# Kernel optimization log

Hardware: AMD Instinct MI355X
Metric: run time of the kernel (lower is better)

The kernel has to match this reference:

```python
import jax, jax.numpy as jnp
import numpy as np

N, E = 50000, 600000
IN, H, C = 128, 8, 32
HC = H * C
LAT, OUT, NCOM = 32, 64, 30
BN_EPS = 1e-5
NEG_SLOPE = 0.2


def setup_inputs() -> dict:
    key = jax.random.key(0)
    ks = jax.random.split(key, 32)
    f32 = jnp.float32
    def rn(i, shape, s=0.05):
        return jax.random.normal(ks[i], shape, f32) * s
    inp = {
        'x': jax.random.normal(ks[0], (N, IN), f32),
        'eps': jax.random.normal(ks[1], (N, LAT), f32),
        'edge_index': jax.random.randint(ks[2], (2, E), 0, N, jnp.int32),
        # GAT layer 1 (in -> H*C)
        'gat1_W': rn(3, (IN, HC)), 'gat1_asrc': rn(4, (H, C)), 'gat1_adst': rn(5, (H, C)), 'gat1_b': jnp.zeros((HC,), f32),
        'bn1_g': jnp.ones((HC,), f32), 'bn1_b': jnp.zeros((HC,), f32),
        # GAT layer 2 (H*C -> H*C)
        'gat2_W': rn(6, (HC, HC)), 'gat2_asrc': rn(7, (H, C)), 'gat2_adst': rn(8, (H, C)), 'gat2_b': jnp.zeros((HC,), f32),
        'bn2_g': jnp.ones((HC,), f32), 'bn2_b': jnp.zeros((HC,), f32),
        # GAT layer 3 (H*C -> H*C)
        'gat3_W': rn(9, (HC, HC)), 'gat3_asrc': rn(10, (H, C)), 'gat3_adst': rn(11, (H, C)), 'gat3_b': jnp.zeros((HC,), f32),
        'bn3_g': jnp.ones((HC,), f32), 'bn3_b': jnp.zeros((HC,), f32),
        # heads
        'res_W': rn(12, (IN, HC)), 'res_b': jnp.zeros((HC,), f32),
        'mu_W': rn(13, (HC, LAT)), 'mu_b': jnp.zeros((LAT,), f32),
        'lv_W': rn(14, (HC, LAT)), 'lv_b': jnp.zeros((LAT,), f32),
        'dec_W': rn(15, (LAT, OUT)), 'dec_b': jnp.zeros((OUT,), f32),
        'aux_W': rn(16, (HC, NCOM)), 'aux_b': jnp.zeros((NCOM,), f32),
    }
    return inp


def gat_conv(x, src, dst, W, asrc, adst, b):
    # PyG GATConv (concat=True, self-loops already in src/dst, lin bias=False)
    n = x.shape[0]
    h = (x @ W).reshape(n, H, C)                      # [N,H,C]
    a_s = jnp.einsum('nhc,hc->nh', h, asrc)           # [N,H]
    a_d = jnp.einsum('nhc,hc->nh', h, adst)
    e = jax.nn.leaky_relu(a_s[src] + a_d[dst], NEG_SLOPE)  # [E,H]
    m = jax.ops.segment_max(e, dst, num_segments=n)        # per-dest softmax (stable)
    p = jnp.exp(e - m[dst])
    s = jax.ops.segment_sum(p, dst, num_segments=n)
    alpha = p / (s[dst] + 1e-16)                      # [E,H]
    out = jax.ops.segment_sum(h[src] * alpha[:, :, None], dst, num_segments=n)
    return out.reshape(n, HC) + b


def batch_norm(x, g, b):
    mu = x.mean(0)
    var = x.var(0)  # biased var, as torch BN uses for normalization
    return (x - mu) * jax.lax.rsqrt(var + BN_EPS) * g + b


def reference(x, eps, edge_index,
              gat1_W, gat1_asrc, gat1_adst, gat1_b, bn1_g, bn1_b,
              gat2_W, gat2_asrc, gat2_adst, gat2_b, bn2_g, bn2_b,
              gat3_W, gat3_asrc, gat3_adst, gat3_b, bn3_g, bn3_b,
              res_W, res_b, mu_W, mu_b, lv_W, lv_b, dec_W, dec_b, aux_W, aux_b):
    loops = jnp.arange(N, dtype=edge_index.dtype)
    src = jnp.concatenate([edge_index[0], loops])
    dst = jnp.concatenate([edge_index[1], loops])

    residual = x @ res_W + res_b
    h = jax.nn.relu(batch_norm(gat_conv(x, src, dst, gat1_W, gat1_asrc, gat1_adst, gat1_b), bn1_g, bn1_b))
    h = jax.nn.relu(batch_norm(gat_conv(h, src, dst, gat2_W, gat2_asrc, gat2_adst, gat2_b), bn2_g, bn2_b))
    h = jax.nn.relu(batch_norm(gat_conv(h, src, dst, gat3_W, gat3_asrc, gat3_adst, gat3_b), bn3_g, bn3_b))
    h = h + residual

    mu = h @ mu_W + mu_b
    logvar = h @ lv_W + lv_b
    z = mu + eps * jnp.exp(0.5 * logvar)   # reparameterize
    out = z @ dec_W + dec_b
    aux = h @ aux_W + aux_b
    return (out, mu, logvar, aux)
```

## Files before the change

### kernel.cpp

```cpp
#include <hip/hip_runtime.h>

#define N_NODES 50000
#define N_EDGES 600000
#define HC 256
#define NH 8
#define AGG_BLOCKS 2048
#define AGG_WAVES (AGG_BLOCKS * 4)

typedef short s8v __attribute__((ext_vector_type(8)));
typedef float f4v __attribute__((ext_vector_type(4)));
typedef _Float16 h4v __attribute__((ext_vector_type(4)));
typedef __attribute__((address_space(1))) const unsigned int as1_cu32;
typedef __attribute__((address_space(3))) unsigned int as3_u32;

__device__ inline ushort f2bf(float f) {
  unsigned u = __float_as_uint(f);
  unsigned r = u + 0x7FFF + ((u >> 16) & 1);
  return (ushort)(r >> 16);
}

__global__ void k_init_cnt(int* __restrict__ cnt) {
  int i = blockIdx.x * 256 + threadIdx.x;
  if (i < N_NODES) cnt[i] = 1;
}

__global__ void k_count(const int* __restrict__ dstE, int* __restrict__ cnt) {
  int e = blockIdx.x * 256 + threadIdx.x;
  if (e < N_EDGES) atomicAdd(&cnt[dstE[e]], 1);
}

__global__ void k_scan_bsum(const int* __restrict__ cnt, int* __restrict__ bsum) {
  __shared__ int sd[256];
  int i = blockIdx.x * 256 + threadIdx.x;
  sd[threadIdx.x] = (i < N_NODES) ? cnt[i] : 0;
  __syncthreads();
  for (int o = 128; o > 0; o >>= 1) {
    if (threadIdx.x < o) sd[threadIdx.x] += sd[threadIdx.x + o];
    __syncthreads();
  }
  if (threadIdx.x == 0) bsum[blockIdx.x] = sd[0];
}

__global__ void k_scan_offsets(int* __restrict__ bsum, int nb) {
  __shared__ int s[256];
  int t = threadIdx.x;
  int v = (t < nb) ? bsum[t] : 0;
  s[t] = v; __syncthreads();
  for (int o = 1; o < 256; o <<= 1) {
    int x = (t >= o) ? s[t - o] : 0;
    __syncthreads();
    s[t] += x;
    __syncthreads();
  }
  if (t < nb) bsum[t] = s[t] - v;
}

__global__ void k_scan_write(const int* __restrict__ cnt, const int* __restrict__ bsum,
                             int* __restrict__ rowptr, int* __restrict__ fillptr) {
  __shared__ int s[256];
  int t = threadIdx.x;
  int i = blockIdx.x * 256 + t;
  int v = (i < N_NODES) ? cnt[i] : 0;
  s[t] = v; __syncthreads();
  for (int o = 1; o < 256; o <<= 1) {
    int x = (t >= o) ? s[t - o] : 0;
    __syncthreads();
    s[t] += x;
    __syncthreads();
  }
  int excl = s[t] - v + bsum[blockIdx.x];
  if (i < N_NODES) {
    rowptr[i] = excl;
    fillptr[i] = excl;
    if (i == N_NODES - 1) rowptr[N_NODES] = excl + v;
  }
}

__global__ void k_fill(const int* __restrict__ srcE, const int* __restrict__ dstE,
                       int* __restrict__ fillptr, int* __restrict__ srcs) {
  int i = blockIdx.x * 256 + threadIdx.x;
  if (i < N_NODES) {
    int pos = atomicAdd(&fillptr[i], 1);
    srcs[pos] = i;
  } else if (i < N_NODES + N_EDGES) {
    int e = i - N_NODES;
    int pos = atomicAdd(&fillptr[dstE[e]], 1);
    srcs[pos] = srcE[e];
  }
}

__global__ void k_cvt_x(const float* __restrict__ X, ushort* __restrict__ Xb) {
  size_t i = ((size_t)blockIdx.x * 256 + threadIdx.x) * 4;
  float4 x4 = *(const float4*)&X[i];
  ushort4 o;
  o.x = f2bf(x4.x); o.y = f2bf(x4.y); o.z = f2bf(x4.z); o.w = f2bf(x4.w);
  *(ushort4*)&Xb[i] = o;
}

__global__ void k_cvt_wt(const float* __restrict__ W, ushort* __restrict__ Wt, int K, int Nw) {
  __shared__ ushort s[32][33];
  int tx = threadIdx.x & 31, ty = threadIdx.x >> 5;
  int k0 = blockIdx.x * 32, n0 = blockIdx.y * 32;
  for (int j = 0; j < 32; j += 8)
    s[ty + j][tx] = f2bf(W[(size_t)(k0 + ty + j) * Nw + n0 + tx]);
  __syncthreads();
  for (int j = 0; j < 32; j += 8)
    Wt[(size_t)(n0 + ty + j) * K + k0 + tx] = s[tx][ty + j];
}

__global__ void k_pack_head(const float* __restrict__ muW, const float* __restrict__ lvW,
                            const float* __restrict__ auxW, ushort* __restrict__ Wth) {
  int n = blockIdx.x;
  int k = threadIdx.x;
  float v = 0.f;
  if (n < 32) v = muW[k * 32 + n];
  else if (n < 64) v = lvW[k * 32 + (n - 32)];
  else if (n < 94) v = auxW[k * 30 + (n - 64)];
  Wth[n * 256 + k] = f2bf(v);
}

template <typename OutT>
__launch_bounds__(256)
__global__ void k_gemm_bf16(const ushort* __restrict__ A, const ushort* __restrict__ Wt,
                            const float* __restrict__ bias, OutT* __restrict__ Out,
                            int M, int K, int ldc) {
  __shared__ __align__(16) ushort As[16 * 512];
  __shared__ __align__(16) ushort Bs[16 * 512];
  int t = threadIdx.x, w = t >> 6, L = t & 63;
  int bm = blockIdx.x * 128, bn = blockIdx.y * 128;
  int lrow = L & 15, lcol = (L >> 4) * 8;

  const ushort* ga[4];
  const ushort* gb[4];
#pragma unroll
  for (int u = 0; u < 4; u++) {
    int i = w * 4 + u;
    int mt = i >> 1, ks = i & 1;
    int arow = bm + mt * 16 + lrow;
    if (arow >= M) arow = M - 1;
    ga[u] = A + (size_t)arow * K + ks * 32 + lcol;
    int brow = bn + mt * 16 + lrow;
    gb[u] = Wt + (size_t)brow * K + ks * 32 + lcol;
  }

  f4v acc[4][4];
  f4v zero = {0.f, 0.f, 0.f, 0.f};
#pragma unroll
  for (int mi = 0; mi < 4; mi++)
#pragma unroll
    for (int ni = 0; ni < 4; ni++) acc[mi][ni] = zero;

  int wm = (w >> 1) * 4;
  int wn = (w & 1) * 4;

  int nk = K >> 6;
  for (int kt = 0; kt < nk; kt++) {
#pragma unroll
    for (int u = 0; u < 4; u++) {
      int i = w * 4 + u;
      __builtin_amdgcn_global_load_lds((as1_cu32*)ga[u], (as3_u32*)&As[i * 512], 16, 0, 0);
      __builtin_amdgcn_global_load_lds((as1_cu32*)gb[u], (as3_u32*)&Bs[i * 512], 16, 0, 0);
      ga[u] += 64; gb[u] += 64;
    }
    __syncthreads();
#pragma unroll
    for (int ks = 0; ks < 2; ks++) {
      s8v af[4], bf[4];
#pragma unroll
      for (int mi = 0; mi < 4; mi++)
        af[mi] = *(const s8v*)&As[(((wm + mi) * 2 + ks) * 64 + L) * 8];
#pragma unroll
      for (int ni = 0; ni < 4; ni++)
        bf[ni] = *(const s8v*)&Bs[(((wn + ni) * 2 + ks) * 64 + L) * 8];
#pragma unroll
      for (int mi = 0; mi < 4; mi++)
#pragma unroll
        for (int ni = 0; ni < 4; ni++)
          acc[mi][ni] = __builtin_amdgcn_mfma_f32_16x16x32_bf16(af[mi], bf[ni], acc[mi][ni], 0, 0, 0);
    }
    __syncthreads();
  }
#pragma unroll
  for (int ni = 0; ni < 4; ni++) {
    int col = bn + (wn + ni) * 16 + (L & 15);
    float bb = bias ? bias[col] : 0.f;
#pragma unroll
    for (int mi = 0; mi < 4; mi++) {
      int rbase = bm + (wm + mi) * 16 + (L >> 4) * 4;
#pragma unroll
      for (int i = 0; i < 4; i++) {
        int r = rbase + i;
        if (r < M) Out[(size_t)r * ldc + col] = (OutT)(acc[mi][ni][i] + bb);
      }
    }
  }
}

__launch_bounds__(256)
__global__ void k_att(const _Float16* __restrict__ B, const float* __restrict__ asrc,
                      const float* __restrict__ adst,
                      float* __restrict__ as_, float* __restrict__ ad_) {
  int wid = (blockIdx.x * 256 + threadIdx.x) >> 6;
  int lane = threadIdx.x & 63;
  h4v x = *(const h4v*)&B[(size_t)wid * 256 + (lane << 2)];
  float4 s4 = *(const float4*)&asrc[lane << 2];
  float4 d4 = *(const float4*)&adst[lane << 2];
  float x0 = (float)x[0], x1 = (float)x[1], x2 = (float)x[2], x3 = (float)x[3];
  float vs = x0 * s4.x + x1 * s4.y + x2 * s4.z + x3 * s4.w;
  float vd = x0 * d4.x + x1 * d4.y + x2 * d4.z + x3 * d4.w;
  vs += __shfl_xor(vs, 1); vs += __shfl_xor(vs, 2); vs += __shfl_xor(vs, 4);
  vd += __shfl_xor(vd, 1); vd += __shfl_xor(vd, 2); vd += __shfl_xor(vd, 4);
  if ((lane & 7) == 0) {
    as_[wid * NH + (lane >> 3)] = vs;
    ad_[wid * NH + (lane >> 3)] = vd;
  }
}

__launch_bounds__(256)
__global__ void k_agg(const int* __restrict__ rowptr, const int* __restrict__ srcs,
                      const float* __restrict__ as_, const float* __restrict__ ad_,
                      const _Float16* __restrict__ B, const float* __restrict__ gb,
                      _Float16* __restrict__ C, float* __restrict__ part,
                      float* __restrict__ stats) {
  __shared__ float ss[4 * 512];
  int t = threadIdx.x;
  if (blockIdx.x == 0) {
    stats[t] = 0.f; stats[t + 256] = 0.f;
  }
  int w = t >> 6, lane = t & 63;
  int h = lane >> 3;
  int cb = lane << 2;
  float4 g4 = *(const float4*)&gb[cb];
  float sts0 = 0.f, sts1 = 0.f, sts2 = 0.f, sts3 = 0.f;
  float stq0 = 0.f, stq1 = 0.f, stq2 = 0.f, stq3 = 0.f;

  for (int n = blockIdx.x * 4 + w; n < N_NODES; n += AGG_WAVES) {
    int beg = rowptr[n], end = rowptr[n + 1];
    float ad_nh = ad_[n * NH + h];
    float ac0 = 0.f, ac1 = 0.f, ac2 = 0.f, ac3 = 0.f, wsum = 0.f;
    int k = beg;
    for (; k + 4 <= end; k += 4) {
      int s0 = srcs[k], s1 = srcs[k + 1], s2 = srcs[k + 2], s3 = srcs[k + 3];
      h4v b0 = *(const h4v*)&B[(size_t)s0 * 256 + cb];
      h4v b1 = *(const h4v*)&B[(size_t)s1 * 256 + cb];
      h4v b2 = *(const h4v*)&B[(size_t)s2 * 256 + cb];
      h4v b3 = *(const h4v*)&B[(size_t)s3 * 256 + cb];
      float e0 = as_[s0 * NH + h] + ad_nh; e0 = e0 > 0.f ? e0 : 0.2f * e0;
      float e1 = as_[s1 * NH + h] + ad_nh; e1 = e1 > 0.f ? e1 : 0.2f * e1;
      float e2 = as_[s2 * NH + h] + ad_nh; e2 = e2 > 0.f ? e2 : 0.2f * e2;
      float e3 = as_[s3 * NH + h] + ad_nh; e3 = e3 > 0.f ? e3 : 0.2f * e3;
      float p0 = __expf(e0), p1 = __expf(e1), p2 = __expf(e2), p3 = __expf(e3);
      wsum += (p0 + p1) + (p2 + p3);
      ac0 += p0 * (float)b0[0] + p1 * (float)b1[0] + p2 * (float)b2[0] + p3 * (float)b3[0];
      ac1 += p0 * (float)b0[1] + p1 * (float)b1[1] + p2 * (float)b2[1] + p3 * (float)b3[1];
      ac2 += p0 * (float)b0[2] + p1 * (float)b1[2] + p2 * (float)b2[2] + p3 * (float)b3[2];
      ac3 += p0 * (float)b0[3] + p1 * (float)b1[3] + p2 * (float)b2[3] + p3 * (float)b3[3];
    }
    for (; k < end; k++) {
      int s = srcs[k];
      h4v b4 = *(const h4v*)&B[(size_t)s * 256 + cb];
      float e = as_[s * NH + h] + ad_nh;
      e = e > 0.f ? e : 0.2f * e;
      float p = __expf(e);
      wsum += p;
      ac0 += p * (float)b4[0]; ac1 += p * (float)b4[1];
      ac2 += p * (float)b4[2]; ac3 += p * (float)b4[3];
    }
    float inv = 1.f / (wsum + 1e-16f);
    float v0 = ac0 * inv + g4.x, v1 = ac1 * inv + g4.y;
    float v2 = ac2 * inv + g4.z, v3 = ac3 * inv + g4.w;
    h4v o; o[0] = (_Float16)v0; o[1] = (_Float16)v1; o[2] = (_Float16)v2; o[3] = (_Float16)v3;
    *(h4v*)&C[(size_t)n * 256 + cb] = o;
    sts0 += v0; stq0 += v0 * v0;
    sts1 += v1; stq1 += v1 * v1;
    sts2 += v2; stq2 += v2 * v2;
    sts3 += v3; stq3 += v3 * v3;
  }
  float* sw = &ss[w * 512];
  sw[cb + 0] = sts0; sw[cb + 1] = sts1; sw[cb + 2] = sts2; sw[cb + 3] = sts3;
  sw[256 + cb + 0] = stq0; sw[256 + cb + 1] = stq1;
  sw[256 + cb + 2] = stq2; sw[256 + cb + 3] = stq3;
  __syncthreads();
  float p0 = ss[t] + ss[512 + t] + ss[1024 + t] + ss[1536 + t];
  float p1 = ss[256 + t] + ss[768 + t] + ss[1280 + t] + ss[1792 + t];
  part[(size_t)blockIdx.x * 512 + t] = p0;
  part[(size_t)blockIdx.x * 512 + 256 + t] = p1;
}

__global__ void k_bn_reduce(const float* __restrict__ part, float* __restrict__ stats) {
  int i = threadIdx.x;
  int base = blockIdx.x * (AGG_BLOCKS / 16);
  float s0 = 0.f, s1 = 0.f;
  for (int b = 0; b < AGG_BLOCKS / 16; b++) {
    s0 += part[(size_t)(base + b) * 512 + i];
    s1 += part[(size_t)(base + b) * 512 + 256 + i];
  }
  atomicAdd(&stats[i], s0);
  atomicAdd(&stats[256 + i], s1);
}

__global__ void k_bn_relu_cvt(const _Float16* __restrict__ X, const float* __restrict__ stats,
                              const float* __restrict__ g, const float* __restrict__ b,
                              const _Float16* __restrict__ resid, ushort* __restrict__ Xb) {
  size_t i = ((size_t)blockIdx.x * 256 + threadIdx.x) * 4;
  int c = (int)(i & 255);
  const float invN = 1.f / (float)N_NODES;
  h4v x4 = *(const h4v*)&X[i];
  float4 s4 = *(const float4*)&stats[c];
  float4 q4 = *(const float4*)&stats[256 + c];
  float4 g4 = *(const float4*)&g[c];
  float4 b4 = *(const float4*)&b[c];
  float m0 = s4.x * invN, m1 = s4.y * invN, m2 = s4.z * invN, m3 = s4.w * invN;
  float v0 = ((float)x4[0] - m0) * rsqrtf(q4.x * invN - m0 * m0 + 1e-5f) * g4.x + b4.x;
  float v1 = ((float)x4[1] - m1) * rsqrtf(q4.y * invN - m1 * m1 + 1e-5f) * g4.y + b4.y;
  float v2 = ((float)x4[2] - m2) * rsqrtf(q4.z * invN - m2 * m2 + 1e-5f) * g4.z + b4.z;
  float v3 = ((float)x4[3] - m3) * rsqrtf(q4.w * invN - m3 * m3 + 1e-5f) * g4.w + b4.w;
  v0 = v0 > 0.f ? v0 : 0.f; v1 = v1 > 0.f ? v1 : 0.f;
  v2 = v2 > 0.f ? v2 : 0.f; v3 = v3 > 0.f ? v3 : 0.f;
  if (resid) {
    h4v r4 = *(const h4v*)&resid[i];
    v0 += (float)r4[0]; v1 += (float)r4[1]; v2 += (float)r4[2]; v3 += (float)r4[3];
  }
  ushort4 ob;
  ob.x = f2bf(v0); ob.y = f2bf(v1); ob.z = f2bf(v2); ob.w = f2bf(v3);
  *(ushort4*)&Xb[i] = ob;
}

__launch_bounds__(256)
__global__ void k_dec(const _Float16* __restrict__ Hd, const float* __restrict__ eps,
                      const float* __restrict__ mub, const float* __restrict__ lvb,
                      const float* __restrict__ auxb,
                      const float* __restrict__ decW, const float* __restrict__ decb,
                      float* __restrict__ out) {
  __shared__ float wsd[2048];
  __shared__ float shz[4][32];
  int t = threadIdx.x;
  for (int i = t; i < 2048; i += 256) wsd[i] = decW[i];
  int w = t >> 6, lane = t & 63;
  int n = blockIdx.x * 4 + w;
  const _Float16* hd = &Hd[(size_t)n * 128];
  if (lane < 32) {
    float mu = (float)hd[lane] + mub[lane];
    float lv = (float)hd[32 + lane] + lvb[lane];
    out[(size_t)N_NODES * 64 + (size_t)n * 32 + lane] = mu;
    out[(size_t)N_NODES * 96 + (size_t)n * 32 + lane] = lv;
    shz[w][lane] = mu + eps[(size_t)n * 32 + lane] * __expf(0.5f * lv);
  } else if (lane < 62) {
    int j = lane - 32;
    out[(size_t)N_NODES * 128 + (size_t)n * 30 + j] = (float)hd[64 + j] + auxb[j];
  }
  __syncthreads();
  float o = decb[lane];
#pragma unroll 8
  for (int k = 0; k < 32; k++) o += shz[w][k] * wsd[k * 64 + lane];
  out[(size_t)n * 64 + lane] = o;
}

extern "C" void kernel_launch(void* const* d_in, const int* in_sizes, int n_in,
                              void* d_out, int out_size, void* d_ws, size_t ws_size,
                              hipStream_t stream) {
  (void)in_sizes; (void)n_in; (void)out_size; (void)ws_size;
  const float* x    = (const float*)d_in[0];
  const float* eps  = (const float*)d_in[1];
  const int*   ei   = (const int*)d_in[2];
  const float* gW[3]    = {(const float*)d_in[3],  (const float*)d_in[9],  (const float*)d_in[15]};
  const float* gasrc[3] = {(const float*)d_in[4],  (const float*)d_in[10], (const float*)d_in[16]};
  const float* gadst[3] = {(const float*)d_in[5],  (const float*)d_in[11], (const float*)d_in[17]};
  const float* gbias[3] = {(const float*)d_in[6],  (const float*)d_in[12], (const float*)d_in[18]};
  const float* bng[3]   = {(const float*)d_in[7],  (const float*)d_in[13], (const float*)d_in[19]};
  const float* bnb[3]   = {(const float*)d_in[8],  (const float*)d_in[14], (const float*)d_in[20]};
  const float* resW = (const float*)d_in[21];
  const float* resb = (const float*)d_in[22];
  const float* muW  = (const float*)d_in[23];
  const float* mub  = (const float*)d_in[24];
  const float* lvW  = (const float*)d_in[25];
  const float* lvb  = (const float*)d_in[26];
  const float* decW = (const float*)d_in[27];
  const float* decb = (const float*)d_in[28];
  const float* auxW = (const float*)d_in[29];
  const float* auxb = (const float*)d_in[30];
  float* out = (float*)d_out;

  char* ws = (char*)d_ws;
  size_t off = 0;
  auto alloc = [&](size_t bytes) -> void* {
    void* p = ws + off;
    off += (bytes + 255) & ~(size_t)255;
    return p;
  };
  _Float16* X0  = (_Float16*)alloc((size_t)N_NODES * HC * 2);
  _Float16* X1  = (_Float16*)alloc((size_t)N_NODES * HC * 2);
  _Float16* Rr  = (_Float16*)alloc((size_t)N_NODES * HC * 2);
  _Float16* Hd  = (_Float16*)alloc((size_t)N_NODES * 128 * 2);
  ushort* Xb    = (ushort*)alloc((size_t)N_NODES * HC * 2);
  float*  as_   = (float*)alloc((size_t)N_NODES * NH * 4);
  float*  ad_   = (float*)alloc((size_t)N_NODES * NH * 4);
  float*  stats = (float*)alloc(512 * 4);
  float*  part  = (float*)alloc((size_t)AGG_BLOCKS * 512 * 4);
  int* cnt      = (int*)alloc((size_t)N_NODES * 4);
  int* rowptr   = (int*)alloc((size_t)(N_NODES + 1) * 4);
  int* fillptr  = (int*)alloc((size_t)N_NODES * 4);
  int* srcs     = (int*)alloc((size_t)(N_NODES + N_EDGES) * 4);
  int* bsum     = (int*)alloc(256 * 4);
  ushort* Wt1   = (ushort*)alloc(256 * 128 * 2);
  ushort* Wt2   = (ushort*)alloc(256 * 256 * 2);
  ushort* Wt3   = (ushort*)alloc(256 * 256 * 2);
  ushort* WtR   = (ushort*)alloc(256 * 128 * 2);
  ushort* Wth   = (ushort*)alloc(128 * 256 * 2);

  const int NB = (N_NODES + 255) / 256;
  k_init_cnt<<<NB, 256, 0, stream>>>(cnt);
  k_count<<<(N_EDGES + 255) / 256, 256, 0, stream>>>(ei + N_EDGES, cnt);
  k_scan_bsum<<<NB, 256, 0, stream>>>(cnt, bsum);
  k_scan_offsets<<<1, 256, 0, stream>>>(bsum, NB);
  k_scan_write<<<NB, 256, 0, stream>>>(cnt, bsum, rowptr, fillptr);
  k_fill<<<(N_NODES + N_EDGES + 255) / 256, 256, 0, stream>>>(ei, ei + N_EDGES, fillptr, srcs);

  k_cvt_wt<<<dim3(4, 8), 256, 0, stream>>>(gW[0], Wt1, 128, 256);
  k_cvt_wt<<<dim3(8, 8), 256, 0, stream>>>(gW[1], Wt2, 256, 256);
  k_cvt_wt<<<dim3(8, 8), 256, 0, stream>>>(gW[2], Wt3, 256, 256);
  k_cvt_wt<<<dim3(4, 8), 256, 0, stream>>>(resW, WtR, 128, 256);
  k_pack_head<<<128, 256, 0, stream>>>(muW, lvW, auxW, Wth);
  k_cvt_x<<<(N_NODES * 128) / 1024, 256, 0, stream>>>(x, Xb);

  const int GM = (N_NODES + 127) / 128;
  k_gemm_bf16<_Float16><<<dim3(GM, 2), 256, 0, stream>>>(Xb, WtR, resb, Rr, N_NODES, 128, 256);

  const ushort* Wts[3] = {Wt1, Wt2, Wt3};
  int K = 128;
  for (int L = 0; L < 3; L++) {
    k_gemm_bf16<_Float16><<<dim3(GM, 2), 256, 0, stream>>>(Xb, Wts[L], nullptr, X0, N_NODES, K, 256);
    k_att<<<N_NODES / 4, 256, 0, stream>>>(X0, gasrc[L], gadst[L], as_, ad_);
    k_agg<<<AGG_BLOCKS, 256, 0, stream>>>(rowptr, srcs, as_, ad_, X0, gbias[L], X1, part, stats);
    k_bn_reduce<<<16, 256, 0, stream>>>(part, stats);
    k_bn_relu_cvt<<<(N_NODES * HC) / 1024, 256, 0, stream>>>(
        X1, stats, bng[L], bnb[L], (L == 2) ? Rr : nullptr, Xb);
    K = 256;
  }
  k_gemm_bf16<_Float16><<<dim3(GM, 1), 256, 0, stream>>>(Xb, Wth, nullptr, Hd, N_NODES, 256, 128);
  k_dec<<<N_NODES / 4, 256, 0, stream>>>(Hd, eps, mub, lvb, auxb, decW, decb, out);
}
```

Measured before the change: 653.4 us.

## Cooperatively compute edge softmax weights across lanes, broadcast via readlane/shuffle in GAT aggregation

The aggregation loop now processes 8 edges at a time. Each lane loads one (edge, head) source index and attention score, computes its exp weight once, then shares the source index with readlane and the weight with a shuffle. Before, every lane redundantly loaded srcs and as_ and computed exp for each edge. The fp16-to-fp32 multiply-accumulate also uses inline v_fma_mix_f32 instead of separate converts. In exchange it adds cross-lane traffic, a masked tail path, and inline asm that may block compiler scheduling.

```diff
diff --git a/kernel.cpp b/kernel.cpp
--- a/kernel.cpp
+++ b/kernel.cpp
@@ -229,6 +229,8 @@
   }
   int w = t >> 6, lane = t & 63;
   int h = lane >> 3;
+  int j = lane >> 3;
+  int hh = lane & 7;
   int cb = lane << 2;
   float4 g4 = *(const float4*)&gb[cb];
   float sts0 = 0.f, sts1 = 0.f, sts2 = 0.f, sts3 = 0.f;
@@ -236,35 +238,54 @@
 
   for (int n = blockIdx.x * 4 + w; n < N_NODES; n += AGG_WAVES) {
     int beg = rowptr[n], end = rowptr[n + 1];
-    float ad_nh = ad_[n * NH + h];
+    float ad_h = ad_[n * NH + hh];
     float ac0 = 0.f, ac1 = 0.f, ac2 = 0.f, ac3 = 0.f, wsum = 0.f;
     int k = beg;
-    for (; k + 4 <= end; k += 4) {
-      int s0 = srcs[k], s1 = srcs[k + 1], s2 = srcs[k + 2], s3 = srcs[k + 3];
-      h4v b0 = *(const h4v*)&B[(size_t)s0 * 256 + cb];
-      h4v b1 = *(const h4v*)&B[(size_t)s1 * 256 + cb];
-      h4v b2 = *(const h4v*)&B[(size_t)s2 * 256 + cb];
-      h4v b3 = *(const h4v*)&B[(size_t)s3 * 256 + cb];
-      float e0 = as_[s0 * NH + h] + ad_nh; e0 = e0 > 0.f ? e0 : 0.2f * e0;
-      float e1 = as_[s1 * NH + h] + ad_nh; e1 = e1 > 0.f ? e1 : 0.2f * e1;
-      float e2 = as_[s2 * NH + h] + ad_nh; e2 = e2 > 0.f ? e2 : 0.2f * e2;
-      float e3 = as_[s3 * NH + h] + ad_nh; e3 = e3 > 0.f ? e3 : 0.2f * e3;
-      float p0 = __expf(e0), p1 = __expf(e1), p2 = __expf(e2), p3 = __expf(e3);
-      wsum += (p0 + p1) + (p2 + p3);
-      ac0 += p0 * (float)b0[0] + p1 * (float)b1[0] + p2 * (float)b2[0] + p3 * (float)b3[0];
-      ac1 += p0 * (float)b0[1] + p1 * (float)b1[1] + p2 * (float)b2[1] + p3 * (float)b3[1];
-      ac2 += p0 * (float)b0[2] + p1 * (float)b1[2] + p2 * (float)b2[2] + p3 * (float)b3[2];
-      ac3 += p0 * (float)b0[3] + p1 * (float)b1[3] + p2 * (float)b2[3] + p3 * (float)b3[3];
-    }
-    for (; k < end; k++) {
-      int s = srcs[k];
-      h4v b4 = *(const h4v*)&B[(size_t)s * 256 + cb];
-      float e = as_[s * NH + h] + ad_nh;
+    for (; k + 8 <= end; k += 8) {
+      int s = srcs[k + j];
+      float e = as_[s * NH + hh] + ad_h;
       e = e > 0.f ? e : 0.2f * e;
       float p = __expf(e);
-      wsum += p;
-      ac0 += p * (float)b4[0]; ac1 += p * (float)b4[1];
-      ac2 += p * (float)b4[2]; ac3 += p * (float)b4[3];
+#pragma unroll
+      for (int jj = 0; jj < 8; jj++) {
+        int sj = __builtin_amdgcn_readlane(s, jj * 8);
+        float pj = __shfl(p, jj * 8 + h);
+        uint2 b2 = *(const uint2*)(B + (size_t)sj * 256 + cb);
+        wsum += pj;
+        asm("v_fma_mix_f32 %0, %1, %2, %0 op_sel:[0,0,0] op_sel_hi:[0,1,0]"
+            : "+v"(ac0) : "v"(pj), "v"(b2.x));
+        asm("v_fma_mix_f32 %0, %1, %2, %0 op_sel:[0,1,0] op_sel_hi:[0,1,0]"
+            : "+v"(ac1) : "v"(pj), "v"(b2.x));
+        asm("v_fma_mix_f32 %0, %1, %2, %0 op_sel:[0,0,0] op_sel_hi:[0,1,0]"
+            : "+v"(ac2) : "v"(pj), "v"(b2.y));
+        asm("v_fma_mix_f32 %0, %1, %2, %0 op_sel:[0,1,0] op_sel_hi:[0,1,0]"
+            : "+v"(ac3) : "v"(pj), "v"(b2.y));
+      }
+    }
+    if (k < end) {
+      int rem = end - k;
+      int idx = k + j; if (idx >= end) idx = end - 1;
+      int s = srcs[idx];
+      float e = as_[s * NH + hh] + ad_h;
+      e = e > 0.f ? e : 0.2f * e;
+      float p = (j < rem) ? __expf(e) : 0.f;
+#pragma unroll
+      for (int jj = 0; jj < 8; jj++) {
+        if (jj < rem) {
+          int sj = __builtin_amdgcn_readlane(s, jj * 8);
+          float pj = __shfl(p, jj * 8 + h);
+          uint2 b2 = *(const uint2*)(B + (size_t)sj * 256 + cb);
+          wsum += pj;
+          asm("v_fma_mix_f32 %0, %1, %2, %0 op_sel:[0,0,0] op_sel_hi:[0,1,0]"
+              : "+v"(ac0) : "v"(pj), "v"(b2.x));
+          asm("v_fma_mix_f32 %0, %1, %2, %0 op_sel:[0,1,0] op_sel_hi:[0,1,0]"
+              : "+v"(ac1) : "v"(pj), "v"(b2.x));
+          asm("v_fma_mix_f32 %0, %1, %2, %0 op_sel:[0,0,0] op_sel_hi:[0,1,0]"
+              : "+v"(ac2) : "v"(pj), "v"(b2.y));
+          asm("v_fma_mix_f32 %0, %1, %2, %0 op_sel:[0,1,0] op_sel_hi:[0,1,0]"
+              : "+v"(ac3) : "v"(pj), "v"(b2.y));
+        }
+      }
     }
     float inv = 1.f / (wsum + 1e-16f);
     float v0 = ac0 * inv + g4.x, v1 = ac1 * inv + g4.y;
```

Result: slower. 680.2 us (+4.1%).

## Precompute per-edge attention exponentials in separate kernel and use fma_mix in aggregation

Applied to the files above, without the earlier changes.

Adds a k_pre kernel that computes leaky-relu and exp attention weights for every edge and head, storing them in an edge-major p32 buffer laid out in groups of four edges. The aggregation loop then loads four weights with one vector load and accumulates with v_fma_mix_f32 inline asm on packed fp16 features, so it no longer converts fp16 to fp32 separately or computes exp inline. The aim is to cut the ALU work and scattered as_ gathers in the latency-bound gather loop. The cost is an extra kernel launch per layer and writing and reading a roughly 21 MB fp32 weight buffer.

```diff
diff --git a/kernel.cpp b/kernel.cpp
--- a/kernel.cpp
+++ b/kernel.cpp
@@ -217,9 +217,44 @@
 }
 
 __launch_bounds__(256)
+__global__ void k_pre(const int* __restrict__ rowptr, const int* __restrict__ srcs,
+                      const float* __restrict__ as_, const float* __restrict__ ad_,
+                      float* __restrict__ p32) {
+  int t = threadIdx.x;
+  int w = t >> 6, lane = t & 63;
+  int h = lane >> 3, j = lane & 7;
+  int jb = j & 4;
+  int jl = j & 3;
+  for (int n = blockIdx.x * 4 + w; n < N_NODES; n += AGG_WAVES) {
+    int beg = rowptr[n], end = rowptr[n + 1];
+    float adh = ad_[n * NH + h];
+    for (int k = beg; k + 4 <= end; k += 8) {
+      if (k + jb + 4 <= end) {
+        int e = k + j;
+        int s = srcs[e];
+        float v = as_[s * NH + h] + adh;
+        v = v > 0.f ? v : 0.2f * v;
+        p32[(size_t)8 * (k + jb) + h * 4 + jl] = __expf(v);
+      }
+    }
+  }
+}
+
+#define FMA4(P, B2)                                                                        \
+  asm("v_fma_mix_f32 %0, %1, %2, %0 op_sel:[0,0,0] op_sel_hi:[0,1,0]"                      \
+      : "+v"(ac0) : "v"(P), "v"((B2).x));                                                  \
+  asm("v_fma_mix_f32 %0, %1, %2, %0 op_sel:[0,1,0] op_sel_hi:[0,1,0]"                      \
+      : "+v"(ac1) : "v"(P), "v"((B2).x));                                                  \
+  asm("v_fma_mix_f32 %0, %1, %2, %0 op_sel:[0,0,0] op_sel_hi:[0,1,0]"                      \
+      : "+v"(ac2) : "v"(P), "v"((B2).y));                                                  \
+  asm("v_fma_mix_f32 %0, %1, %2, %0 op_sel:[0,1,0] op_sel_hi:[0,1,0]"                      \
+      : "+v"(ac3) : "v"(P), "v"((B2).y));
+
+__launch_bounds__(256)
 __global__ void k_agg(const int* __restrict__ rowptr, const int* __restrict__ srcs,
                       const float* __restrict__ as_, const float* __restrict__ ad_,
-                      const _Float16* __restrict__ B, const float* __restrict__ gb,
+                      const float* __restrict__ p32, const _Float16* __restrict__ B,
+                      const float* __restrict__ gb,
                       _Float16* __restrict__ C, float* __restrict__ part,
                       float* __restrict__ stats) {
   __shared__ float ss[4 * 512];
@@ -230,6 +265,7 @@
   int w = t >> 6, lane = t & 63;
   int h = lane >> 3;
   int cb = lane << 2;
+  const uint2* Bu = (const uint2*)B;
   float4 g4 = *(const float4*)&gb[cb];
   float sts0 = 0.f, sts1 = 0.f, sts2 = 0.f, sts3 = 0.f;
   float stq0 = 0.f, stq1 = 0.f, stq2 = 0.f, stq3 = 0.f;
@@ -238,23 +274,20 @@
     int beg = rowptr[n], end = rowptr[n + 1];
     float ad_nh = ad_[n * NH + h];
     float ac0 = 0.f, ac1 = 0.f, ac2 = 0.f, ac3 = 0.f, wsum = 0.f;
+    f4v wv = {0.f, 0.f, 0.f, 0.f};
     int k = beg;
     for (; k + 4 <= end; k += 4) {
+      f4v p4 = *(const f4v*)&p32[(size_t)8 * k + h * 4];
       int s0 = srcs[k], s1 = srcs[k + 1], s2 = srcs[k + 2], s3 = srcs[k + 3];
-      h4v b0 = *(const h4v*)&B[(size_t)s0 * 256 + cb];
-      h4v b1 = *(const h4v*)&B[(size_t)s1 * 256 + cb];
-      h4v b2 = *(const h4v*)&B[(size_t)s2 * 256 + cb];
-      h4v b3 = *(const h4v*)&B[(size_t)s3 * 256 + cb];
-      float e0 = as_[s0 * NH + h] + ad_nh; e0 = e0 > 0.f ? e0 : 0.2f * e0;
-      float e1 = as_[s1 * NH + h] + ad_nh; e1 = e1 > 0.f ? e1 : 0.2f * e1;
-      float e2 = as_[s2 * NH + h] + ad_nh; e2 = e2 > 0.f ? e2 : 0.2f * e2;
-      float e3 = as_[s3 * NH + h] + ad_nh; e3 = e3 > 0.f ? e3 : 0.2f * e3;
-      float p0 = __expf(e0), p1 = __expf(e1), p2 = __expf(e2), p3 = __expf(e3);
-      wsum += (p0 + p1) + (p2 + p3);
-      ac0 += p0 * (float)b0[0] + p1 * (float)b1[0] + p2 * (float)b2[0] + p3 * (float)b3[0];
-      ac1 += p0 * (float)b0[1] + p1 * (float)b1[1] + p2 * (float)b2[1] + p3 * (float)b3[1];
-      ac2 += p0 * (float)b0[2] + p1 * (float)b1[2] + p2 * (float)b2[2] + p3 * (float)b3[2];
-      ac3 += p0 * (float)b0[3] + p1 * (float)b1[3] + p2 * (float)b2[3] + p3 * (float)b3[3];
+      uint2 b0 = Bu[(size_t)s0 * 64 + lane];
+      uint2 b1 = Bu[(size_t)s1 * 64 + lane];
+      uint2 b2 = Bu[(size_t)s2 * 64 + lane];
+      uint2 b3 = Bu[(size_t)s3 * 64 + lane];
+      wv += p4;
+      FMA4(p4[0], b0)
+      FMA4(p4[1], b1)
+      FMA4(p4[2], b2)
+      FMA4(p4[3], b3)
     }
     for (; k < end; k++) {
       int s = srcs[k];
@@ -266,6 +299,7 @@
       ac0 += p * (float)b4[0]; ac1 += p * (float)b4[1];
       ac2 += p * (float)b4[2]; ac3 += p * (float)b4[3];
     }
+    wsum += (wv[0] + wv[1]) + (wv[2] + wv[3]);
     float inv = 1.f / (wsum + 1e-16f);
     float v0 = ac0 * inv + g4.x, v1 = ac1 * inv + g4.y;
     float v2 = ac2 * inv + g4.z, v3 = ac3 * inv + g4.w;
@@ -395,6 +429,7 @@
   ushort* Xb    = (ushort*)alloc((size_t)N_NODES * HC * 2);
   float*  as_   = (float*)alloc((size_t)N_NODES * NH * 4);
   float*  ad_   = (float*)alloc((size_t)N_NODES * NH * 4);
+  float*  p32   = (float*)alloc((size_t)(N_NODES + N_EDGES) * NH * 4);
   float*  stats = (float*)alloc(512 * 4);
   float*  part  = (float*)alloc((size_t)AGG_BLOCKS * 512 * 4);
   int* cnt      = (int*)alloc((size_t)N_NODES * 4);
@@ -431,7 +466,8 @@
   for (int L = 0; L < 3; L++) {
     k_gemm_bf16<_Float16><<<dim3(GM, 2), 256, 0, stream>>>(Xb, Wts[L], nullptr, X0, N_NODES, K, 256);
     k_att<<<N_NODES / 4, 256, 0, stream>>>(X0, gasrc[L], gadst[L], as_, ad_);
-    k_agg<<<AGG_BLOCKS, 256, 0, stream>>>(rowptr, srcs, as_, ad_, X0, gbias[L], X1, part, stats);
+    k_pre<<<AGG_BLOCKS, 256, 0, stream>>>(rowptr, srcs, as_, ad_, p32);
+    k_agg<<<AGG_BLOCKS, 256, 0, stream>>>(rowptr, srcs, as_, ad_, p32, X0, gbias[L], X1, part, stats);
     k_bn_reduce<<<16, 256, 0, stream>>>(part, stats);
     k_bn_relu_cvt<<<(N_NODES * HC) / 1024, 256, 0, stream>>>(
         X1, stats, bng[L], bnb[L], (L == 2) ? Rr : nullptr, Xb);
```

Result: slower. 681.4 us (+4.3%).
